# Performance work log

Measured on AMD Instinct MI355X. Metric: run time of the kernel, lower is better.

## Reference

```python
import jax, jax.numpy as jnp
import numpy as np
from jax import lax

B = 1024        # batch
K = 512         # codebook size
A = 18          # n_actions (Atari full action set)
BETA = 0.25     # commitment loss weight


def _conv(x, w, b, stride):
    # NCHW / OIHW valid conv, as nn.Conv2d with padding=0
    y = lax.conv_general_dilated(x, w, (stride, stride), 'VALID',
                                 dimension_numbers=('NCHW', 'OIHW', 'NCHW'))
    return y + b[None, :, None, None]


def _deconv(x, w, b, stride, k):
    # ConvTranspose2d(padding=0) == conv with lhs_dilation=stride, pad k-1
    y = lax.conv_general_dilated(x, w, (1, 1), [(k - 1, k - 1)] * 2,
                                 lhs_dilation=(stride, stride),
                                 dimension_numbers=('NCHW', 'OIHW', 'NCHW'))
    return y + b[None, :, None, None]


def setup_inputs() -> dict:
    key = jax.random.key(0)
    ks = jax.random.split(key, 20)
    def n(k, shape, s=0.05):
        return jax.random.normal(k, shape, jnp.float32) * s
    return {
        'x':   jax.random.uniform(ks[0], (B, 4, 84, 84), jnp.float32) * 255.0,
        'w1':  n(ks[1], (32, 4, 4, 4)),   'b1': n(ks[2], (32,)),
        'w2':  n(ks[3], (64, 32, 3, 3)),  'b2': n(ks[4], (64,)),
        'w3':  n(ks[5], (64, 64, 3, 3)),  'b3': n(ks[6], (64,)),
        'emb': n(ks[7], (K, 64), 1.0),
        'dw1': n(ks[8], (64, 64, 3, 3)),  'db1': n(ks[9], (64,)),
        'dw2': n(ks[10], (32, 64, 3, 3)), 'db2': n(ks[11], (32,)),
        'dw3': n(ks[12], (4, 32, 4, 4)),  'db3': n(ks[13], (4,)),
        'lw1': n(ks[14], (4096, 512)),    'lb1': n(ks[15], (512,)),
        'lw2': n(ks[16], (512, A)),       'lb2': n(ks[17], (A,)),
    }


def reference(x, w1, b1, w2, b2, w3, b3, emb,
              dw1, db1, dw2, db2, dw3, db3,
              lw1, lb1, lw2, lb2):
    x = x / 255.0                      # forward() scaling
    h = x / 255.0                      # encode() scales again (faithful)
    h = jax.nn.relu(_conv(h, w1, b1, 4))   # [B,32,21,21]
    h = jax.nn.relu(_conv(h, w2, b2, 2))   # [B,64,10,10]
    enc = jax.nn.relu(_conv(h, w3, b3, 1)) # [B,64,8,8]

    # --- VQ codebook lookup ---
    b_, c, hh, ww = enc.shape
    q = enc.transpose(0, 2, 3, 1).reshape(b_, hh * ww, c)      # [B,L,64]
    # squared euclidean distances to codebook (argmin identical to cdist argmin)
    d2 = (jnp.sum(q * q, -1, keepdims=True)
          - 2.0 * jnp.einsum('bld,kd->blk', q, emb)
          + jnp.sum(emb * emb, -1))                             # [B,L,K]
    idx = jnp.argmin(d2, axis=-1)                               # [B,L]
    qo = emb[idx.reshape(-1)]                                   # [B*L,64]
    qi = q.reshape(-1, c)                                       # [B*L,64]

    commitment = jnp.mean((lax.stop_gradient(qo) - qi) ** 2)
    codebook = jnp.mean((qo - lax.stop_gradient(qi)) ** 2)
    quant_loss = codebook + BETA * commitment

    st = qi + lax.stop_gradient(qo - qi)                        # straight-through
    quant = st.reshape(b_, hh, ww, c).transpose(0, 3, 1, 2)     # [B,64,8,8]

    # --- decoder ---
    d = jax.nn.relu(_deconv(quant, dw1, db1, 1, 3))  # [B,64,10,10]
    d = jax.nn.relu(_deconv(d, dw2, db2, 2, 3))      # [B,32,21,21]
    dec = jax.nn.sigmoid(_deconv(d, dw3, db3, 4, 4)) # [B,4,84,84]
    reconstruction_loss = jnp.mean((dec - x) ** 2)

    # --- Q head on detached quantized features ---
    flat = lax.stop_gradient(quant).reshape(b_, -1)             # [B,4096]
    q_values = jax.nn.relu(flat @ lw1 + lb1) @ lw2 + lb2        # [B,A]
    return (q_values, reconstruction_loss, quant_loss)
```

## Files before the change

### kernel.cpp

```cpp
#include <hip/hip_runtime.h>
#include <hip/hip_bf16.h>


#define ENC_SCALE (1.0f/65025.0f)

__global__ __launch_bounds__(256) void zero_k(float* __restrict__ hidden,
                                              float* __restrict__ accum) {
  int t = blockIdx.x * 256 + threadIdx.x;
  if (t < 524288) hidden[t] = 0.f;
  if (t < 8) accum[t] = 0.f;
}

__global__ __launch_bounds__(256) void conv1_k(
    const float* __restrict__ x, const float* __restrict__ w1,
    const float* __restrict__ b1, float* __restrict__ out) {
  int lane = threadIdx.x & 63;
  int wv = __builtin_amdgcn_readfirstlane(threadIdx.x >> 6);
  int oc0 = wv * 8;
  int p = blockIdx.x * 64 + lane;
  int b = p / 441, rem = p % 441;
  int oy = rem / 21, ox = rem % 21;
  const float* xb = x + (long)b * 28224 + (oy * 4) * 84 + ox * 4;
  const float* wp = w1 + oc0 * 64;
  float acc[8];
  #pragma unroll
  for (int c = 0; c < 8; ++c) acc[c] = b1[oc0 + c];
  #pragma unroll 1
  for (int i = 0; i < 4; ++i)
    #pragma unroll
    for (int ky = 0; ky < 4; ++ky)
      #pragma unroll
      for (int kx = 0; kx < 4; ++kx) {
        float v = xb[i * 7056 + ky * 84 + kx] * ENC_SCALE;
        int t = i * 16 + ky * 4 + kx;
        #pragma unroll
        for (int c = 0; c < 8; ++c)
          acc[c] = fmaf(v, wp[c * 64 + t], acc[c]);
      }
  float* ob = out + ((long)b * 32 + oc0) * 441 + rem;
  #pragma unroll
  for (int c = 0; c < 8; ++c) ob[c * 441] = fmaxf(acc[c], 0.f);
}

__global__ __launch_bounds__(256) void conv2_k(
    const float* __restrict__ in, const float* __restrict__ w,
    const float* __restrict__ bias, float* __restrict__ out) {
  __shared__ float in_s[32 * 441];
  int b = blockIdx.x, tid = threadIdx.x;
  const float4* src = (const float4*)(in + (long)b * 14112);
  for (int i = tid; i < 3528; i += 256) *(float4*)&in_s[i * 4] = src[i];
  __syncthreads();
  int lane = tid & 63;
  int wv = __builtin_amdgcn_readfirstlane(tid >> 6);
  int oc0 = wv * 16;
  int pxA = lane;
  int pxB = 64 + lane; if (pxB > 99) pxB = 99;
  int oyA = pxA / 10, oxA = pxA % 10;
  int oyB = pxB / 10, oxB = pxB % 10;
  float accA[16], accB[16];
  #pragma unroll
  for (int o = 0; o < 16; ++o) { float bv = bias[oc0 + o]; accA[o] = bv; accB[o] = bv; }
  #pragma unroll 2
  for (int ic = 0; ic < 32; ++ic) {
    const float* is = in_s + ic * 441;
    float a[9], bb[9];
    #pragma unroll
    for (int ky = 0; ky < 3; ++ky)
      #pragma unroll
      for (int kx = 0; kx < 3; ++kx) {
        a[ky * 3 + kx]  = is[(2 * oyA + ky) * 21 + 2 * oxA + kx];
        bb[ky * 3 + kx] = is[(2 * oyB + ky) * 21 + 2 * oxB + kx];
      }
    #pragma unroll
    for (int o = 0; o < 16; ++o) {
      const float* wp = w + (long)(oc0 + o) * 288 + ic * 9;
      #pragma unroll
      for (int t = 0; t < 9; ++t) {
        float wt = wp[t];
        accA[o] = fmaf(a[t], wt, accA[o]);
        accB[o] = fmaf(bb[t], wt, accB[o]);
      }
    }
  }
  float* ob = out + ((long)b * 64 + oc0) * 100;
  #pragma unroll
  for (int o = 0; o < 16; ++o) {
    ob[o * 100 + pxA] = fmaxf(accA[o], 0.f);
    if (lane < 36) ob[o * 100 + 64 + lane] = fmaxf(accB[o], 0.f);
  }
}

__global__ __launch_bounds__(256) void conv3_k(
    const float* __restrict__ in, const float* __restrict__ w,
    const float* __restrict__ bias, float* __restrict__ out) {
  __shared__ float in_s[6400];
  int b = blockIdx.x, tid = threadIdx.x;
  const float4* src = (const float4*)(in + (long)b * 6400);
  for (int i = tid; i < 1600; i += 256) *(float4*)&in_s[i * 4] = src[i];
  __syncthreads();
  int lane = tid & 63;
  int wv = __builtin_amdgcn_readfirstlane(tid >> 6);
  int oc0 = wv * 16;
  int oy = lane >> 3, ox = lane & 7;
  float acc[16];
  #pragma unroll
  for (int o = 0; o < 16; ++o) acc[o] = bias[oc0 + o];
  #pragma unroll 2
  for (int ic = 0; ic < 64; ++ic) {
    const float* is = in_s + ic * 100;
    float a[9];
    #pragma unroll
    for (int ky = 0; ky < 3; ++ky)
      #pragma unroll
      for (int kx = 0; kx < 3; ++kx)
        a[ky * 3 + kx] = is[(oy + ky) * 10 + ox + kx];
    #pragma unroll
    for (int o = 0; o < 16; ++o) {
      const float* wp = w + (long)(oc0 + o) * 576 + ic * 9;
      #pragma unroll
      for (int t = 0; t < 9; ++t) acc[o] = fmaf(a[t], wp[t], acc[o]);
    }
  }
  float* ob = out + ((long)b * 64 + oc0) * 64 + lane;
  #pragma unroll
  for (int o = 0; o < 16; ++o) ob[o * 64] = fmaxf(acc[o], 0.f);
}

__global__ __launch_bounds__(256) void vq_k(
    const float* __restrict__ enc, const float* __restrict__ emb,
    float* __restrict__ quant, float* __restrict__ vqpart) {
  __shared__ float elT[64 * 516];
  __shared__ float qT[64 * 36];
  __shared__ float qq_s[32];
  __shared__ float ee_s[512];
  __shared__ float lsum[4];

  int tid = threadIdx.x;
  int b = blockIdx.x;
  int lane = tid & 63;
  int w = tid >> 6;

  for (int s = tid; s < 512 * 64; s += 256) {
    int k = s >> 6, d = s & 63;
    elT[d * 516 + k] = emb[s];
  }
  __syncthreads();
  for (int kk = tid; kk < 512; kk += 256) {
    float s = 0.f;
    for (int d = 0; d < 64; ++d) { float e = elT[d * 516 + kk]; s = fmaf(e, e, s); }
    ee_s[kk] = s;
  }
  __syncthreads();
  float eer[8];
  #pragma unroll
  for (int j = 0; j < 2; ++j)
    #pragma unroll
    for (int c = 0; c < 4; ++c) eer[j * 4 + c] = ee_s[j * 256 + lane * 4 + c];

  float lossacc = 0.f;
  for (int pass = 0; pass < 2; ++pass) {
    int l0 = pass * 32;
    __syncthreads();
    for (int s = tid; s < 2048; s += 256) {
      int r = s & 31, d = s >> 5;
      qT[d * 36 + r] = enc[((b * 64 + d) << 6) + l0 + r];
    }
    __syncthreads();
    if (tid < 32) {
      float s = 0.f;
      for (int d = 0; d < 64; ++d) { float v = qT[d * 36 + tid]; s = fmaf(v, v, s); }
      qq_s[tid] = s;
    }
    __syncthreads();

    int r0 = w * 8;
    float dot[8][8] = {};
    #pragma unroll 2
    for (int d = 0; d < 64; ++d) {
      float4 e0 = *(const float4*)&elT[d * 516 + lane * 4];
      float4 e1 = *(const float4*)&elT[d * 516 + 256 + lane * 4];
      float4 q0 = *(const float4*)&qT[d * 36 + r0];
      float4 q1 = *(const float4*)&qT[d * 36 + r0 + 4];
      float qv[8] = {q0.x, q0.y, q0.z, q0.w, q1.x, q1.y, q1.z, q1.w};
      float ev[8] = {e0.x, e0.y, e0.z, e0.w, e1.x, e1.y, e1.z, e1.w};
      #pragma unroll
      for (int r = 0; r < 8; ++r)
        #pragma unroll
        for (int je = 0; je < 8; ++je)
          dot[r][je] = fmaf(qv[r], ev[je], dot[r][je]);
    }

    #pragma unroll 1
    for (int r = 0; r < 8; ++r) {
      float best = 1e30f; int bk = 0;
      #pragma unroll
      for (int je = 0; je < 8; ++je) {
        float sc = fmaf(-2.f, dot[r][je], eer[je]);
        int k = (je >> 2) * 256 + lane * 4 + (je & 3);
        if (sc < best || (sc == best && k < bk)) { best = sc; bk = k; }
      }
      #pragma unroll
      for (int off = 32; off; off >>= 1) {
        float ob = __shfl_xor(best, off);
        int ok = __shfl_xor(bk, off);
        if (ob < best || (ob == best && ok < bk)) { best = ob; bk = ok; }
      }
      int l = l0 + r0 + r;
      quant[((b << 6) + lane) * 64 + l] = emb[bk * 64 + lane];
      if (lane == 0) lossacc += qq_s[r0 + r] + best;
    }
  }
  if (lane == 0) lsum[w] = lossacc;
  __syncthreads();
  if (tid == 0) vqpart[b] = lsum[0] + lsum[1] + lsum[2] + lsum[3];
}

__global__ __launch_bounds__(256) void dec1_k(
    const float* __restrict__ in, const float* __restrict__ w,
    const float* __restrict__ bias, float* __restrict__ out) {
  __shared__ float in_s[64 * 144];
  int b = blockIdx.x, tid = threadIdx.x;
  for (int i = tid; i < 9216; i += 256) in_s[i] = 0.f;
  __syncthreads();
  const float* src = in + (long)b * 4096;
  for (int i = tid; i < 4096; i += 256) {
    int ic = i >> 6, p = i & 63;
    in_s[ic * 144 + (2 + (p >> 3)) * 12 + 2 + (p & 7)] = src[i];
  }
  __syncthreads();
  int lane = tid & 63;
  int wv = __builtin_amdgcn_readfirstlane(tid >> 6);
  int oc0 = wv * 16;
  int pxA = lane;
  int pxB = 64 + lane; if (pxB > 99) pxB = 99;
  int oyA = pxA / 10, oxA = pxA % 10;
  int oyB = pxB / 10, oxB = pxB % 10;
  float accA[16], accB[16];
  #pragma unroll
  for (int o = 0; o < 16; ++o) { float bv = bias[oc0 + o]; accA[o] = bv; accB[o] = bv; }
  #pragma unroll 2
  for (int ic = 0; ic < 64; ++ic) {
    const float* is = in_s + ic * 144;
    float a[9], bb[9];
    #pragma unroll
    for (int ky = 0; ky < 3; ++ky)
      #pragma unroll
      for (int kx = 0; kx < 3; ++kx) {
        a[ky * 3 + kx]  = is[(oyA + ky) * 12 + oxA + kx];
        bb[ky * 3 + kx] = is[(oyB + ky) * 12 + oxB + kx];
      }
    #pragma unroll
    for (int o = 0; o < 16; ++o) {
      const float* wp = w + (long)(oc0 + o) * 576 + ic * 9;
      #pragma unroll
      for (int t = 0; t < 9; ++t) {
        float wt = wp[t];
        accA[o] = fmaf(a[t], wt, accA[o]);
        accB[o] = fmaf(bb[t], wt, accB[o]);
      }
    }
  }
  float* ob = out + ((long)b * 64 + oc0) * 100;
  #pragma unroll
  for (int o = 0; o < 16; ++o) {
    ob[o * 100 + pxA] = fmaxf(accA[o], 0.f);
    if (lane < 36) ob[o * 100 + 64 + lane] = fmaxf(accB[o], 0.f);
  }
}

__global__ __launch_bounds__(256) void dec2_k(
    const float* __restrict__ in, const float* __restrict__ w,
    const float* __restrict__ bias, float* __restrict__ out) {
  __shared__ float in_s[64 * 144];
  int b = blockIdx.x, tid = threadIdx.x;
  for (int i = tid; i < 9216; i += 256) in_s[i] = 0.f;
  __syncthreads();
  const float* src = in + (long)b * 6400;
  for (int i = tid; i < 6400; i += 256) {
    int ic = i / 100, p = i % 100;
    in_s[ic * 144 + (p / 10) * 12 + (p % 10)] = src[i];
  }
  __syncthreads();
  int lane = tid & 63;
  int wv = __builtin_amdgcn_readfirstlane(tid >> 6);
  int oc0 = wv * 8;
  float* ob = out + ((long)b * 32 + oc0) * 441;
  float bias8[8];
  #pragma unroll
  for (int o = 0; o < 8; ++o) bias8[o] = bias[oc0 + o];

  #pragma unroll 1
  for (int pp = 0; pp < 2; ++pp) {
    int idx = pp * 64 + lane; bool okl = idx < 121; int ii = okl ? idx : 0;
    int u = ii / 11, v = ii % 11;
    float acc[8];
    #pragma unroll
    for (int o = 0; o < 8; ++o) acc[o] = bias8[o];
    #pragma unroll 2
    for (int ic = 0; ic < 64; ++ic) {
      const float* is = in_s + ic * 144;
      float i00 = is[(u + 1) * 12 + v + 1];
      float i02 = is[(u + 1) * 12 + v];
      float i20 = is[u * 12 + v + 1];
      float i22 = is[u * 12 + v];
      #pragma unroll
      for (int o = 0; o < 8; ++o) {
        const float* wp = w + (long)(oc0 + o) * 576 + ic * 9;
        acc[o] = fmaf(i00, wp[0], acc[o]);
        acc[o] = fmaf(i02, wp[2], acc[o]);
        acc[o] = fmaf(i20, wp[6], acc[o]);
        acc[o] = fmaf(i22, wp[8], acc[o]);
      }
    }
    if (okl) {
      int off = (2 * u) * 21 + 2 * v;
      #pragma unroll
      for (int o = 0; o < 8; ++o) ob[o * 441 + off] = fmaxf(acc[o], 0.f);
    }
  }
  #pragma unroll 1
  for (int pp = 0; pp < 2; ++pp) {
    int idx = pp * 64 + lane; bool okl = idx < 110; int ii = okl ? idx : 0;
    int u = ii / 10, v = ii % 10;
    float acc[8];
    #pragma unroll
    for (int o = 0; o < 8; ++o) acc[o] = bias8[o];
    #pragma unroll 2
    for (int ic = 0; ic < 64; ++ic) {
      const float* is = in_s + ic * 144;
      float i0 = is[(u + 1) * 12 + v + 1];
      float i2 = is[u * 12 + v + 1];
      #pragma unroll
      for (int o = 0; o < 8; ++o) {
        const float* wp = w + (long)(oc0 + o) * 576 + ic * 9;
        acc[o] = fmaf(i0, wp[1], acc[o]);
        acc[o] = fmaf(i2, wp[7], acc[o]);
      }
    }
    if (okl) {
      int off = (2 * u) * 21 + 2 * v + 1;
      #pragma unroll
      for (int o = 0; o < 8; ++o) ob[o * 441 + off] = fmaxf(acc[o], 0.f);
    }
  }
  #pragma unroll 1
  for (int pp = 0; pp < 2; ++pp) {
    int idx = pp * 64 + lane; bool okl = idx < 110; int ii = okl ? idx : 0;
    int u = ii / 11, v = ii % 11;
    float acc[8];
    #pragma unroll
    for (int o = 0; o < 8; ++o) acc[o] = bias8[o];
    #pragma unroll 2
    for (int ic = 0; ic < 64; ++ic) {
      const float* is = in_s + ic * 144;
      float i0 = is[(u + 1) * 12 + v + 1];
      float i2 = is[(u + 1) * 12 + v];
      #pragma unroll
      for (int o = 0; o < 8; ++o) {
        const float* wp = w + (long)(oc0 + o) * 576 + ic * 9;
        acc[o] = fmaf(i0, wp[3], acc[o]);
        acc[o] = fmaf(i2, wp[5], acc[o]);
      }
    }
    if (okl) {
      int off = (2 * u + 1) * 21 + 2 * v;
      #pragma unroll
      for (int o = 0; o < 8; ++o) ob[o * 441 + off] = fmaxf(acc[o], 0.f);
    }
  }
  #pragma unroll 1
  for (int pp = 0; pp < 2; ++pp) {
    int idx = pp * 64 + lane; bool okl = idx < 100; int ii = okl ? idx : 0;
    int u = ii / 10, v = ii % 10;
    float acc[8];
    #pragma unroll
    for (int o = 0; o < 8; ++o) acc[o] = bias8[o];
    #pragma unroll 2
    for (int ic = 0; ic < 64; ++ic) {
      const float* is = in_s + ic * 144;
      float i0 = is[(u + 1) * 12 + v + 1];
      #pragma unroll
      for (int o = 0; o < 8; ++o) {
        const float* wp = w + (long)(oc0 + o) * 576 + ic * 9;
        acc[o] = fmaf(i0, wp[4], acc[o]);
      }
    }
    if (okl) {
      int off = (2 * u + 1) * 21 + 2 * v + 1;
      #pragma unroll
      for (int o = 0; o < 8; ++o) ob[o * 441 + off] = fmaxf(acc[o], 0.f);
    }
  }
}

__global__ __launch_bounds__(256) void dec3_k(
    const float* __restrict__ d2, const float* __restrict__ dw3,
    const float* __restrict__ db3, const float* __restrict__ x,
    float* __restrict__ part) {
  int t = blockIdx.x * 256 + threadIdx.x;
  int b = t / 441, r = t % 441;
  int ty = r / 21, tx = r % 21;
  const float* ib = d2 + (long)b * 14112 + ty * 21 + tx;
  float acc[4][4][4];
  #pragma unroll
  for (int c = 0; c < 4; ++c) {
    float bv = db3[c];
    #pragma unroll
    for (int ry = 0; ry < 4; ++ry)
      #pragma unroll
      for (int rx = 0; rx < 4; ++rx) acc[c][ry][rx] = bv;
  }
  #pragma unroll 4
  for (int i = 0; i < 32; ++i) {
    float v = ib[i * 441];
    #pragma unroll
    for (int c = 0; c < 4; ++c) {
      const float* wp = dw3 + (c * 32 + i) * 16;
      #pragma unroll
      for (int ky = 0; ky < 4; ++ky) {
        float4 wv = *(const float4*)(wp + ky * 4);
        int ry = 3 - ky;
        acc[c][ry][3] = fmaf(v, wv.x, acc[c][ry][3]);
        acc[c][ry][2] = fmaf(v, wv.y, acc[c][ry][2]);
        acc[c][ry][1] = fmaf(v, wv.z, acc[c][ry][1]);
        acc[c][ry][0] = fmaf(v, wv.w, acc[c][ry][0]);
      }
    }
  }
  int y0 = ty * 4, x0 = tx * 4;
  const float* xb = x + (long)b * 28224 + y0 * 84 + x0;
  float ls = 0.f;
  #pragma unroll
  for (int c = 0; c < 4; ++c)
    #pragma unroll
    for (int ry = 0; ry < 4; ++ry) {
      float4 xv = *(const float4*)(xb + c * 7056 + ry * 84);
      float xs[4] = {xv.x, xv.y, xv.z, xv.w};
      #pragma unroll
      for (int rx = 0; rx < 4; ++rx) {
        float dec = 1.f / (1.f + __expf(-acc[c][ry][rx]));
        float df = dec - xs[rx] * (1.f / 255.f);
        ls = fmaf(df, df, ls);
      }
    }
  #pragma unroll
  for (int off = 32; off; off >>= 1) ls += __shfl_down(ls, off);
  __shared__ float r4[4];
  if ((threadIdx.x & 63) == 0) r4[threadIdx.x >> 6] = ls;
  __syncthreads();
  if (threadIdx.x == 0) part[blockIdx.x] = r4[0] + r4[1] + r4[2] + r4[3];
}

__global__ __launch_bounds__(256) void reduce_k(
    const float* __restrict__ dec3part, const float* __restrict__ vqpart,
    float* __restrict__ accum) {
  int tid = threadIdx.x;
  float s0 = 0.f, s1 = 0.f;
  for (int i = tid; i < 1764; i += 256) s0 += dec3part[i];
  for (int i = tid; i < 1024; i += 256) s1 += vqpart[i];
  #pragma unroll
  for (int off = 32; off; off >>= 1) {
    s0 += __shfl_down(s0, off);
    s1 += __shfl_down(s1, off);
  }
  __shared__ float a0[4], a1[4];
  int lane = tid & 63, w = tid >> 6;
  if (lane == 0) { a0[w] = s0; a1[w] = s1; }
  __syncthreads();
  if (tid == 0) {
    accum[0] = a0[0] + a0[1] + a0[2] + a0[3];
    accum[1] = a1[0] + a1[1] + a1[2] + a1[3];
  }
}

__global__ __launch_bounds__(256) void fc1_k(
    const float* __restrict__ quant, const float* __restrict__ lw1,
    float* __restrict__ hidden) {
  int n = (blockIdx.x & 1) * 256 + threadIdx.x;
  int bg = (blockIdx.x >> 1) & 63;
  int ks = blockIdx.x >> 7;
  int b0 = bg * 16;
  const float* q0 = quant + (long)b0 * 4096 + ks * 1024;
  const float* w0 = lw1 + (long)ks * 1024 * 512 + n;
  float acc[16] = {};
  #pragma unroll 4
  for (int k = 0; k < 1024; ++k) {
    float wvv = w0[(long)k * 512];
    #pragma unroll
    for (int bb = 0; bb < 16; ++bb)
      acc[bb] = fmaf(q0[bb * 4096 + k], wvv, acc[bb]);
  }
  #pragma unroll
  for (int bb = 0; bb < 16; ++bb)
    atomicAdd(&hidden[(b0 + bb) * 512 + n], acc[bb]);
}

__global__ __launch_bounds__(256) void fc2_k(
    const float* __restrict__ hidden, const float* __restrict__ lb1,
    const float* __restrict__ lw2, const float* __restrict__ lb2,
    const float* __restrict__ accum, float* __restrict__ out) {
  int t = blockIdx.x * 256 + threadIdx.x;
  int b = t / 18, a = t % 18;
  const float* h = hidden + b * 512;
  float acc = lb2[a];
  #pragma unroll 4
  for (int n = 0; n < 512; ++n) {
    float hv = fmaxf(h[n] + lb1[n], 0.f);
    acc = fmaf(hv, lw2[n * 18 + a], acc);
  }
  out[t] = acc;
  if (t == 0) {
    out[18432] = accum[0] * (1.f / 28901376.f);
    out[18433] = 1.25f * accum[1] * (1.f / 4194304.f);
  }
}

extern "C" void kernel_launch(void* const* d_in, const int* in_sizes, int n_in,
                              void* d_out, int out_size, void* d_ws, size_t ws_size,
                              hipStream_t stream) {
  const float* x   = (const float*)d_in[0];
  const float* w1  = (const float*)d_in[1];
  const float* b1  = (const float*)d_in[2];
  const float* w2  = (const float*)d_in[3];
  const float* b2  = (const float*)d_in[4];
  const float* w3  = (const float*)d_in[5];
  const float* b3  = (const float*)d_in[6];
  const float* emb = (const float*)d_in[7];
  const float* dw1 = (const float*)d_in[8];
  const float* db1 = (const float*)d_in[9];
  const float* dw2 = (const float*)d_in[10];
  const float* db2 = (const float*)d_in[11];
  const float* dw3 = (const float*)d_in[12];
  const float* db3 = (const float*)d_in[13];
  const float* lw1 = (const float*)d_in[14];
  const float* lb1 = (const float*)d_in[15];
  const float* lw2 = (const float*)d_in[16];
  const float* lb2 = (const float*)d_in[17];

  float* ws = (float*)d_ws;
  float* h1     = ws;
  float* h2     = ws + 14450688;
  float* enc    = ws + 21004288;
  float* quant  = ws + 25198592;
  float* d1     = h2;
  float* d2b    = h1;
  float* hidden = ws + 29392896;
  float* accum  = ws + 29917184;
  float* d3part = ws + 29917192;
  float* vqpart = ws + 29918956;
  float* outp   = (float*)d_out;

  zero_k<<<2048, 256, 0, stream>>>(hidden, accum);
  conv1_k<<<dim3(7056, 1), 256, 0, stream>>>(x, w1, b1, h1);
  conv2_k<<<1024, 256, 0, stream>>>(h1, w2, b2, h2);
  conv3_k<<<1024, 256, 0, stream>>>(h2, w3, b3, enc);
  vq_k<<<1024, 256, 0, stream>>>(enc, emb, quant, vqpart);
  dec1_k<<<1024, 256, 0, stream>>>(quant, dw1, db1, d1);
  dec2_k<<<1024, 256, 0, stream>>>(d1, dw2, db2, d2b);
  dec3_k<<<1764, 256, 0, stream>>>(d2b, dw3, db3, x, d3part);
  reduce_k<<<1, 256, 0, stream>>>(d3part, vqpart, accum);
  fc1_k<<<512, 256, 0, stream>>>(quant, lw1, hidden);
  fc2_k<<<72, 256, 0, stream>>>(hidden, lb1, lw2, lb2, accum, outp);
}
```

Baseline: 1.222 ms.

## Rewrite VQ kernel as one thread per position with register-held query

The VQ lookup kernel no longer stages the whole transposed codebook in LDS for every block. Each thread now holds one position's 64-dim query in registers and scans all 512 codebook entries, reading embeddings through uniform global loads. Four batches are handled per block, so the launch shrinks to 256 blocks and the partial-loss reduction is adjusted to match. This removes the heavy per-block LDS fill and transpose of the codebook. In exchange, 64 registers per thread may lower occupancy, and every thread streams the full codebook from cache with little reuse across the block, serialising 512×64 FMAs per thread.

```diff
diff --git a/kernel.cpp b/kernel.cpp
--- a/kernel.cpp
+++ b/kernel.cpp
@@ -129,90 +129,46 @@
 __global__ __launch_bounds__(256) void vq_k(
     const float* __restrict__ enc, const float* __restrict__ emb,
     float* __restrict__ quant, float* __restrict__ vqpart) {
-  __shared__ float elT[64 * 516];
-  __shared__ float qT[64 * 36];
-  __shared__ float qq_s[32];
   __shared__ float ee_s[512];
   __shared__ float lsum[4];
-
   int tid = threadIdx.x;
-  int b = blockIdx.x;
-  int lane = tid & 63;
-  int w = tid >> 6;
-
-  for (int s = tid; s < 512 * 64; s += 256) {
-    int k = s >> 6, d = s & 63;
-    elT[d * 516 + k] = emb[s];
-  }
-  __syncthreads();
-  for (int kk = tid; kk < 512; kk += 256) {
+  for (int k = tid; k < 512; k += 256) {
+    const float* ep = emb + k * 64;
     float s = 0.f;
-    for (int d = 0; d < 64; ++d) { float e = elT[d * 516 + kk]; s = fmaf(e, e, s); }
-    ee_s[kk] = s;
-  }
-  __syncthreads();
-  float eer[8];
-  #pragma unroll
-  for (int j = 0; j < 2; ++j)
-    #pragma unroll
-    for (int c = 0; c < 4; ++c) eer[j * 4 + c] = ee_s[j * 256 + lane * 4 + c];
-
-  float lossacc = 0.f;
-  for (int pass = 0; pass < 2; ++pass) {
-    int l0 = pass * 32;
-    __syncthreads();
-    for (int s = tid; s < 2048; s += 256) {
-      int r = s & 31, d = s >> 5;
-      qT[d * 36 + r] = enc[((b * 64 + d) << 6) + l0 + r];
-    }
-    __syncthreads();
-    if (tid < 32) {
-      float s = 0.f;
-      for (int d = 0; d < 64; ++d) { float v = qT[d * 36 + tid]; s = fmaf(v, v, s); }
-      qq_s[tid] = s;
-    }
-    __syncthreads();
-
-    int r0 = w * 8;
-    float dot[8][8] = {};
-    #pragma unroll 2
-    for (int d = 0; d < 64; ++d) {
-      float4 e0 = *(const float4*)&elT[d * 516 + lane * 4];
-      float4 e1 = *(const float4*)&elT[d * 516 + 256 + lane * 4];
-      float4 q0 = *(const float4*)&qT[d * 36 + r0];
-      float4 q1 = *(const float4*)&qT[d * 36 + r0 + 4];
-      float qv[8] = {q0.x, q0.y, q0.z, q0.w, q1.x, q1.y, q1.z, q1.w};
-      float ev[8] = {e0.x, e0.y, e0.z, e0.w, e1.x, e1.y, e1.z, e1.w};
-      #pragma unroll
-      for (int r = 0; r < 8; ++r)
-        #pragma unroll
-        for (int je = 0; je < 8; ++je)
-          dot[r][je] = fmaf(qv[r], ev[je], dot[r][je]);
-    }
-
-    #pragma unroll 1
-    for (int r = 0; r < 8; ++r) {
-      float best = 1e30f; int bk = 0;
-      #pragma unroll
-      for (int je = 0; je < 8; ++je) {
-        float sc = fmaf(-2.f, dot[r][je], eer[je]);
-        int k = (je >> 2) * 256 + lane * 4 + (je & 3);
-        if (sc < best || (sc == best && k < bk)) { best = sc; bk = k; }
-      }
-      #pragma unroll
-      for (int off = 32; off; off >>= 1) {
-        float ob = __shfl_xor(best, off);
-        int ok = __shfl_xor(bk, off);
-        if (ob < best || (ob == best && ok < bk)) { best = ob; bk = ok; }
-      }
-      int l = l0 + r0 + r;
-      quant[((b << 6) + lane) * 64 + l] = emb[bk * 64 + lane];
-      if (lane == 0) lossacc += qq_s[r0 + r] + best;
-    }
-  }
-  if (lane == 0) lsum[w] = lossacc;
-  __syncthreads();
-  if (tid == 0) vqpart[b] = lsum[0] + lsum[1] + lsum[2] + lsum[3];
+    #pragma unroll
+    for (int d = 0; d < 64; ++d) s = fmaf(ep[d], ep[d], s);
+    ee_s[k] = s;
+  }
+  __syncthreads();
+  int w = tid >> 6, lane = tid & 63;
+  int b = blockIdx.x * 4 + w;
+  const float* qb = enc + ((long)b << 12) + lane;
+  float q[64];
+  #pragma unroll
+  for (int d = 0; d < 64; ++d) q[d] = qb[d << 6];
+  float qq = 0.f;
+  #pragma unroll
+  for (int d = 0; d < 64; ++d) qq = fmaf(q[d], q[d], qq);
+  float best = 1e30f; int bk = 0;
+  #pragma unroll 4
+  for (int k = 0; k < 512; ++k) {
+    const float* ep = emb + (k << 6);
+    float dot = 0.f;
+    #pragma unroll
+    for (int d = 0; d < 64; ++d) dot = fmaf(q[d], ep[d], dot);
+    float sc = fmaf(-2.f, dot, ee_s[k]);
+    if (sc < best) { best = sc; bk = k; }
+  }
+  float* qo = quant + ((long)b << 12) + lane;
+  const float* eb = emb + (bk << 6);
+  #pragma unroll 8
+  for (int d = 0; d < 64; ++d) qo[d << 6] = eb[d];
+  float ls = qq + best;
+  #pragma unroll
+  for (int off = 32; off; off >>= 1) ls += __shfl_down(ls, off);
+  if (lane == 0) lsum[w] = ls;
+  __syncthreads();
+  if (tid == 0) vqpart[blockIdx.x] = lsum[0] + lsum[1] + lsum[2] + lsum[3];
 }
 
 __global__ __launch_bounds__(256) void dec1_k(
@@ -457,7 +413,7 @@
   int tid = threadIdx.x;
   float s0 = 0.f, s1 = 0.f;
   for (int i = tid; i < 1764; i += 256) s0 += dec3part[i];
-  for (int i = tid; i < 1024; i += 256) s1 += vqpart[i];
+  if (tid < 256) s1 = vqpart[tid];
   #pragma unroll
   for (int off = 32; off; off >>= 1) {
     s0 += __shfl_down(s0, off);
@@ -554,7 +510,7 @@
   conv1_k<<<dim3(7056, 1), 256, 0, stream>>>(x, w1, b1, h1);
   conv2_k<<<1024, 256, 0, stream>>>(h1, w2, b2, h2);
   conv3_k<<<1024, 256, 0, stream>>>(h2, w3, b3, enc);
-  vq_k<<<1024, 256, 0, stream>>>(enc, emb, quant, vqpart);
+  vq_k<<<256, 256, 0, stream>>>(enc, emb, quant, vqpart);
   dec1_k<<<1024, 256, 0, stream>>>(quant, dw1, db1, d1);
   dec2_k<<<1024, 256, 0, stream>>>(d1, dw2, db2, d2b);
   dec3_k<<<1764, 256, 0, stream>>>(d2b, dw3, db3, x, d3part);
```

New measurement: 1.260 ms. 1.03x slower.
